# Performance work log

Hardware: AMD Instinct MI355X
Metric: run time of the kernel (lower is better)

Reference implementation:

```python
import jax, jax.numpy as jnp
import numpy as np


def _up(x, h, w):
    # bicubic (Keys a=-0.5, matching PIL BICUBIC) resize of [B,H,W] -> [B,h,w]
    return jax.image.resize(x, (x.shape[0], h, w), method='cubic')


def setup_inputs() -> dict:
    key = jax.random.key(0)
    ks = jax.random.split(key, 10)
    B = 64
    inp = {
        'cam_256': jax.random.uniform(ks[0], (B, 256, 256), dtype=jnp.float32),
        'cam_128': jax.random.uniform(ks[1], (B, 128, 128), dtype=jnp.float32),
        'cam_64':  jax.random.uniform(ks[2], (B, 64, 64), dtype=jnp.float32),
        'cam_32':  jax.random.uniform(ks[3], (B, 32, 32), dtype=jnp.float32),
        'w1': jax.random.normal(ks[4], (2,), dtype=jnp.float32),
        'b1': jax.random.normal(ks[5], (1,), dtype=jnp.float32),
        'w2': jax.random.normal(ks[6], (2,), dtype=jnp.float32),
        'b2': jax.random.normal(ks[7], (1,), dtype=jnp.float32),
        'w3': jax.random.normal(ks[8], (2,), dtype=jnp.float32),
        'b3': jax.random.normal(ks[9], (1,), dtype=jnp.float32),
    }
    return inp


def reference(cam_256, cam_128, cam_64, cam_32, w1, b1, w2, b2, w3, b3):
    B = cam_32.shape[0]
    # stage 1: up(32->64), concat with cam_64, 1x1 conv(2->1) + ReLU
    up32 = _up(cam_32, 64, 64)                              # [B,64,64]
    h64 = jax.nn.relu(w1[0] * up32 + w1[1] * cam_64 + b1[0])
    # stage 2: up(64->128), concat with cam_128, 1x1 conv + ReLU
    up64 = _up(h64, 128, 128)
    h128 = jax.nn.relu(w2[0] * up64 + w2[1] * cam_128 + b2[0])
    # stage 3: up(128->256), concat with cam_256, 1x1 conv + ReLU
    up128 = _up(h128, 256, 256)
    h256 = jax.nn.relu(w3[0] * up128 + w3[1] * cam_256 + b3[0])
    # final: bicubic up to 1024; original loop prepends each new image,
    # reversing batch order -> replicate with flip
    out = _up(h256, 1024, 1024)                             # [B,1024,1024]
    out = jnp.flip(out, axis=0)[:, None]                    # [B,1,1024,1024]
    return out
```

## Files before the change

### kernel.cpp

```cpp
#include <hip/hip_runtime.h>

typedef float vfloat4 __attribute__((ext_vector_type(4)));
typedef float vfloat2 __attribute__((ext_vector_type(2)));

template <bool B> struct BoolC { static constexpr bool value = B; };

__device__ __forceinline__ int iclamp(int v, int lo, int hi) {
  return v < lo ? lo : (v > hi ? hi : v);
}

__device__ __forceinline__ void taps4w(int i, int n, float inv, float w[4]) {
  float s = ((float)i + 0.5f) * inv - 0.5f;
  int k0 = (int)floorf(s);
  float sum = 0.f;
#pragma unroll
  for (int t = 0; t < 4; ++t) {
    int j = k0 - 1 + t;
    float d = fabsf(s - (float)j);
    float wt = (d <= 1.f) ? (((1.5f * d - 2.5f) * d) * d + 1.f)
                          : (((-0.5f * d + 2.5f) * d - 4.f) * d + 2.f);
    if (j < 0 || j >= n) wt = 0.f;
    w[t] = wt;
    sum += wt;
  }
  float r = 1.f / sum;
#pragma unroll
  for (int t = 0; t < 4; ++t) w[t] *= r;
}

#define W0_0 (-0.0439453125f)
#define W0_1 ( 0.3896484375f)
#define W0_2 ( 0.7275390625f)
#define W0_3 (-0.0732421875f)
#define W1_0 (-0.0068359375f)
#define W1_1 ( 0.0908203125f)
#define W1_2 ( 0.9638671875f)
#define W1_3 (-0.0478515625f)
#define U_0 (-0.0234375f)
#define U_1 ( 0.2265625f)
#define U_2 ( 0.8671875f)
#define U_3 (-0.0703125f)

__device__ __forceinline__ void up2_cell(const float (&f)[5][5], int k, int g, int n,
                                         float (&o)[2][2]) {
  if (g >= 2 && g <= n - 3 && k >= 2 && k <= n - 3) {
    float v0[5], v1[5];
#pragma unroll
    for (int c = 0; c < 5; ++c) {
      v0[c] = U_0 * f[0][c] + U_1 * f[1][c] + U_2 * f[2][c] + U_3 * f[3][c];
      v1[c] = U_3 * f[1][c] + U_2 * f[2][c] + U_1 * f[3][c] + U_0 * f[4][c];
    }
    o[0][0] = U_0 * v0[0] + U_1 * v0[1] + U_2 * v0[2] + U_3 * v0[3];
    o[0][1] = U_3 * v0[1] + U_2 * v0[2] + U_1 * v0[3] + U_0 * v0[4];
    o[1][0] = U_0 * v1[0] + U_1 * v1[1] + U_2 * v1[2] + U_3 * v1[3];
    o[1][1] = U_3 * v1[1] + U_2 * v1[2] + U_1 * v1[3] + U_0 * v1[4];
  } else {
#pragma unroll
    for (int p = 0; p < 2; ++p) {
      float wy[4];
      taps4w(2 * k + p, n, 0.5f, wy);
      float vv[5];
#pragma unroll
      for (int c = 0; c < 5; ++c)
        vv[c] = wy[0] * f[p][c] + wy[1] * f[p + 1][c] + wy[2] * f[p + 2][c] + wy[3] * f[p + 3][c];
#pragma unroll
      for (int q = 0; q < 2; ++q) {
        float wx[4];
        taps4w(2 * g + q, n, 0.5f, wx);
        o[p][q] = wx[0] * vv[q] + wx[1] * vv[q + 1] + wx[2] * vv[q + 2] + wx[3] * vv[q + 3];
      }
    }
  }
}

__global__ void __launch_bounds__(256, 4) fused_all(
    const float* __restrict__ cam256, const float* __restrict__ cam128,
    const float* __restrict__ cam64, const float* __restrict__ cam32,
    const float* __restrict__ w1, const float* __restrict__ b1,
    const float* __restrict__ w2, const float* __restrict__ b2,
    const float* __restrict__ w3, const float* __restrict__ b3,
    float* __restrict__ out) {
  __shared__ float s_h64[12 * 64];
  __shared__ float s_h128[16 * 128];
  __shared__ float s_h256[20 * 256];

  const int tid = threadIdx.x;
  const int slab = blockIdx.x;
  const int b = blockIdx.y;
  const int s = slab * 16;

  const int r_lo = s - 2 < 0 ? 0 : s - 2, r_hi = s + 17 > 255 ? 255 : s + 17;
  const int kr0 = r_lo >> 1, kr1 = r_hi >> 1;
  const int h256_row0 = 2 * kr0;
  const int j_lo = kr0 - 2 < 0 ? 0 : kr0 - 2, j_hi = kr1 + 2 > 127 ? 127 : kr1 + 2;
  const int kj0 = j_lo >> 1, kj1 = j_hi >> 1;
  const int h128_row0 = 2 * kj0;
  const int m_lo = kj0 - 2 < 0 ? 0 : kj0 - 2, m_hi = kj1 + 2 > 63 ? 63 : kj1 + 2;
  const int km0 = m_lo >> 1, km1 = m_hi >> 1;
  const int h64_row0 = 2 * km0;

  const float w1_0 = w1[0], w1_1 = w1[1], b1_0 = b1[0];
  const float w2_0 = w2[0], w2_1 = w2[1], b2_0 = b2[0];
  const float w3_0 = w3[0], w3_1 = w3[1], b3_0 = b3[0];

  {
    const float* c32 = cam32 + (size_t)b * 32 * 32;
    const float* c64 = cam64 + (size_t)b * 64 * 64;
    const int nk = km1 - km0 + 1;
    for (int idx = tid; idx < nk * 32; idx += 256) {
      int k = km0 + (idx >> 5), g = idx & 31;
      float f[5][5];
#pragma unroll
      for (int i = 0; i < 5; ++i) {
        int r = iclamp(k - 2 + i, 0, 31);
#pragma unroll
        for (int c = 0; c < 5; ++c) f[i][c] = c32[r * 32 + iclamp(g - 2 + c, 0, 31)];
      }
      float o[2][2];
      up2_cell(f, k, g, 32, o);
#pragma unroll
      for (int p = 0; p < 2; ++p)
#pragma unroll
        for (int q = 0; q < 2; ++q) {
          int row = 2 * k + p, col = 2 * g + q;
          float h = w1_0 * o[p][q] + w1_1 * c64[row * 64 + col] + b1_0;
          s_h64[(row - h64_row0) * 64 + col] = fmaxf(h, 0.f);
        }
    }
  }
  __syncthreads();

  {
    const float* c128 = cam128 + (size_t)b * 128 * 128;
    const int nk = kj1 - kj0 + 1;
    for (int idx = tid; idx < nk * 64; idx += 256) {
      int k = kj0 + (idx >> 6), g = idx & 63;
      float f[5][5];
#pragma unroll
      for (int i = 0; i < 5; ++i) {
        int r = iclamp(k - 2 + i, 0, 63) - h64_row0;
#pragma unroll
        for (int c = 0; c < 5; ++c) f[i][c] = s_h64[r * 64 + iclamp(g - 2 + c, 0, 63)];
      }
      float o[2][2];
      up2_cell(f, k, g, 64, o);
#pragma unroll
      for (int p = 0; p < 2; ++p)
#pragma unroll
        for (int q = 0; q < 2; ++q) {
          int row = 2 * k + p, col = 2 * g + q;
          float h = w2_0 * o[p][q] + w2_1 * c128[row * 128 + col] + b2_0;
          s_h128[(row - h128_row0) * 128 + col] = fmaxf(h, 0.f);
        }
    }
  }
  __syncthreads();

  {
    const float* c256 = cam256 + (size_t)b * 256 * 256;
    const int gc = tid & 127;
    const int sub = tid >> 7;
    const int nk = kr1 - kr0 + 1;
    const int len = (nk + 1) >> 1;
    const int ks = kr0 + sub * len;
    int ke = ks + len - 1;
    if (ke > kr1) ke = kr1;
    if (ks <= kr1) {
      const int cc0 = iclamp(gc - 2, 0, 127), cc1 = iclamp(gc - 1, 0, 127), cc2 = gc,
                cc3 = iclamp(gc + 1, 0, 127), cc4 = iclamp(gc + 2, 0, 127);
      float wa0, wa1, wa2, wa3, wb0, wb1, wb2, wb3;
      if (gc >= 2 && gc <= 125) {
        wa0 = U_0; wa1 = U_1; wa2 = U_2; wa3 = U_3;
        wb0 = U_3; wb1 = U_2; wb2 = U_1; wb3 = U_0;
      } else {
        float ta[4], tb[4];
        taps4w(2 * gc, 128, 0.5f, ta);
        taps4w(2 * gc + 1, 128, 0.5f, tb);
        wa0 = ta[0]; wa1 = ta[1]; wa2 = ta[2]; wa3 = ta[3];
        wb0 = tb[0]; wb1 = tb[1]; wb2 = tb[2]; wb3 = tb[3];
      }
#define H128_ROW_HX(RCLAMP, DST)                                                \
      {                                                                         \
        const float* rp_ = s_h128 + ((RCLAMP) - h128_row0) * 128;               \
        float f0_ = rp_[cc0], f1_ = rp_[cc1], f2_ = rp_[cc2], f3_ = rp_[cc3],   \
              f4_ = rp_[cc4];                                                   \
        DST[0] = wa0 * f0_ + wa1 * f1_ + wa2 * f2_ + wa3 * f3_;                 \
        DST[1] = wb0 * f1_ + wb1 * f2_ + wb2 * f3_ + wb3 * f4_;                 \
      }
      float hx[5][2];
#pragma unroll
      for (int w = 0; w < 5; ++w) {
        int rc = iclamp(ks - 2 + w, 0, 127);
        H128_ROW_HX(rc, hx[w]);
      }
      for (int k = ks; k <= ke; ++k) {
        if (k > ks) {
#pragma unroll
          for (int w = 0; w < 4; ++w) { hx[w][0] = hx[w + 1][0]; hx[w][1] = hx[w + 1][1]; }
          int rc = iclamp(k + 2, 0, 127);
          H128_ROW_HX(rc, hx[4]);
        }
        float p0w[4], p1w[4];
        if (k < 2 || k > 125) {
          taps4w(2 * k, 128, 0.5f, p0w);
          taps4w(2 * k + 1, 128, 0.5f, p1w);
        } else {
          p0w[0] = U_0; p0w[1] = U_1; p0w[2] = U_2; p0w[3] = U_3;
          p1w[0] = U_3; p1w[1] = U_2; p1w[2] = U_1; p1w[3] = U_0;
        }
        float o00 = p0w[0] * hx[0][0] + p0w[1] * hx[1][0] + p0w[2] * hx[2][0] + p0w[3] * hx[3][0];
        float o01 = p0w[0] * hx[0][1] + p0w[1] * hx[1][1] + p0w[2] * hx[2][1] + p0w[3] * hx[3][1];
        float o10 = p1w[0] * hx[1][0] + p1w[1] * hx[2][0] + p1w[2] * hx[3][0] + p1w[3] * hx[4][0];
        float o11 = p1w[0] * hx[1][1] + p1w[1] * hx[2][1] + p1w[2] * hx[3][1] + p1w[3] * hx[4][1];
        const int row0 = 2 * k, col = 2 * gc;
        vfloat2 ca = *(const vfloat2*)(c256 + (size_t)row0 * 256 + col);
        vfloat2 cb = *(const vfloat2*)(c256 + (size_t)(row0 + 1) * 256 + col);
        vfloat2 h0 = {fmaxf(w3_0 * o00 + w3_1 * ca.x + b3_0, 0.f),
                      fmaxf(w3_0 * o01 + w3_1 * ca.y + b3_0, 0.f)};
        vfloat2 h1 = {fmaxf(w3_0 * o10 + w3_1 * cb.x + b3_0, 0.f),
                      fmaxf(w3_0 * o11 + w3_1 * cb.y + b3_0, 0.f)};
        *(vfloat2*)(&s_h256[(row0 - h256_row0) * 256 + col]) = h0;
        *(vfloat2*)(&s_h256[(row0 + 1 - h256_row0) * 256 + col]) = h1;
      }
#undef H128_ROW_HX
    }
  }
  __syncthreads();

  {
    float* outimg = out + (size_t)(63 - b) * 1024 * 1024;
    const int g = tid;
    const int kbase = s;
    const int cc0 = iclamp(g - 2, 0, 255), cc1 = iclamp(g - 1, 0, 255), cc2 = g,
              cc3 = iclamp(g + 1, 0, 255), cc4 = iclamp(g + 2, 0, 255);
    float wx00, wx01, wx02, wx03, wx10, wx11, wx12, wx13;
    float wx20, wx21, wx22, wx23, wx30, wx31, wx32, wx33;
    if (g >= 2 && g <= 253) {
      wx00 = W0_0; wx01 = W0_1; wx02 = W0_2; wx03 = W0_3;
      wx10 = W1_0; wx11 = W1_1; wx12 = W1_2; wx13 = W1_3;
      wx20 = W1_3; wx21 = W1_2; wx22 = W1_1; wx23 = W1_0;
      wx30 = W0_3; wx31 = W0_2; wx32 = W0_1; wx33 = W0_0;
    } else {
      float t0[4], t1[4], t2[4], t3[4];
      taps4w(4 * g + 0, 256, 0.25f, t0);
      taps4w(4 * g + 1, 256, 0.25f, t1);
      taps4w(4 * g + 2, 256, 0.25f, t2);
      taps4w(4 * g + 3, 256, 0.25f, t3);
      wx00 = t0[0]; wx01 = t0[1]; wx02 = t0[2]; wx03 = t0[3];
      wx10 = t1[0]; wx11 = t1[1]; wx12 = t1[2]; wx13 = t1[3];
      wx20 = t2[0]; wx21 = t2[1]; wx22 = t2[2]; wx23 = t2[3];
      wx30 = t3[0]; wx31 = t3[1]; wx32 = t3[2]; wx33 = t3[3];
    }
#define H256_ROW_HX(RCLAMP, DST)                                                \
    {                                                                           \
      const float* rp_ = s_h256 + ((RCLAMP) - h256_row0) * 256;                 \
      float f0_ = rp_[cc0], f1_ = rp_[cc1], f2_ = rp_[cc2], f3_ = rp_[cc3],     \
            f4_ = rp_[cc4];                                                     \
      DST[0] = wx00 * f0_ + wx01 * f1_ + wx02 * f2_ + wx03 * f3_;               \
      DST[1] = wx10 * f0_ + wx11 * f1_ + wx12 * f2_ + wx13 * f3_;               \
      DST[2] = wx20 * f1_ + wx21 * f2_ + wx22 * f3_ + wx23 * f4_;               \
      DST[3] = wx30 * f1_ + wx31 * f2_ + wx32 * f3_ + wx33 * f4_;               \
    }
    auto phaseD = [&](auto bndc) {
      constexpr bool BND = decltype(bndc)::value;
      float hx[5][4];
#pragma unroll
      for (int w = 0; w < 5; ++w) {
        int rc = iclamp(kbase - 2 + w, 0, 255);
        H256_ROW_HX(rc, hx[w]);
      }
      float* op = outimg + (size_t)4 * kbase * 1024 + 4 * g;
#pragma unroll
      for (int step = 0; step < 16; ++step) {
        const int k = kbase + step;
        if (step) {
#pragma unroll
          for (int w = 0; w < 4; ++w)
#pragma unroll
            for (int q = 0; q < 4; ++q) hx[w][q] = hx[w + 1][q];
          int rc = iclamp(k + 2, 0, 255);
          H256_ROW_HX(rc, hx[4]);
        }
        float wy0[4], wy1[4], wy2[4], wy3[4];
        const bool maybe_bnd = BND && ((step < 2) || (step >= 14));
        if (maybe_bnd && (k < 2 || k > 253)) {
          taps4w(4 * k + 0, 256, 0.25f, wy0);
          taps4w(4 * k + 1, 256, 0.25f, wy1);
          taps4w(4 * k + 2, 256, 0.25f, wy2);
          taps4w(4 * k + 3, 256, 0.25f, wy3);
        } else {
          wy0[0] = W0_0; wy0[1] = W0_1; wy0[2] = W0_2; wy0[3] = W0_3;
          wy1[0] = W1_0; wy1[1] = W1_1; wy1[2] = W1_2; wy1[3] = W1_3;
          wy2[0] = W1_3; wy2[1] = W1_2; wy2[2] = W1_1; wy2[3] = W1_0;
          wy3[0] = W0_3; wy3[1] = W0_2; wy3[2] = W0_1; wy3[3] = W0_0;
        }
        vfloat4 v0, v1, v2, v3;
#pragma unroll
        for (int q = 0; q < 4; ++q) {
          v0[q] = wy0[0] * hx[0][q] + wy0[1] * hx[1][q] + wy0[2] * hx[2][q] + wy0[3] * hx[3][q];
          v1[q] = wy1[0] * hx[0][q] + wy1[1] * hx[1][q] + wy1[2] * hx[2][q] + wy1[3] * hx[3][q];
          v2[q] = wy2[0] * hx[1][q] + wy2[1] * hx[2][q] + wy2[2] * hx[3][q] + wy2[3] * hx[4][q];
          v3[q] = wy3[0] * hx[1][q] + wy3[1] * hx[2][q] + wy3[2] * hx[3][q] + wy3[3] * hx[4][q];
        }
        float* rp = op + (size_t)step * 4096;
        *(vfloat4*)(rp) = v0;
        *(vfloat4*)(rp + 1024) = v1;
        *(vfloat4*)(rp + 2048) = v2;
        *(vfloat4*)(rp + 3072) = v3;
      }
    };
    if (slab == 0 || slab == 15) phaseD(BoolC<true>{});
    else phaseD(BoolC<false>{});
#undef H256_ROW_HX
  }
}

extern "C" void kernel_launch(void* const* d_in, const int* in_sizes, int n_in_,
                              void* d_out, int out_size, void* d_ws, size_t ws_size,
                              hipStream_t stream) {
  const float* cam256 = (const float*)d_in[0];
  const float* cam128 = (const float*)d_in[1];
  const float* cam64  = (const float*)d_in[2];
  const float* cam32  = (const float*)d_in[3];
  const float* w1 = (const float*)d_in[4];
  const float* b1 = (const float*)d_in[5];
  const float* w2 = (const float*)d_in[6];
  const float* b2 = (const float*)d_in[7];
  const float* w3 = (const float*)d_in[8];
  const float* b3 = (const float*)d_in[9];
  float* out = (float*)d_out;

  fused_all<<<dim3(16, 64), 256, 0, stream>>>(cam256, cam128, cam64, cam32,
                                              w1, b1, w2, b2, w3, b3, out);
}
```

Measured before the change: 296.0 us.

## Split fused pyramid kernel into h256 producer and streaming 4x upsample kernel

Splits the single fused kernel into two launches. The first computes the 256x256 intermediate per image slab and writes it to workspace. The second streams the final 4x bicubic upsample with a much larger grid (64x64 blocks), reading h256 from global memory and writing vector float4 output rows. This aims to improve parallelism and store bandwidth for the dominant 1024x1024 output write. It costs an extra 16MB round trip and a second launch, and it falls back to the fused kernel when no workspace is provided.

```diff
diff --git a/kernel.cpp b/kernel.cpp
--- a/kernel.cpp
+++ b/kernel.cpp
@@ -71,6 +71,244 @@
       }
     }
   }
+}
+
+__global__ void __launch_bounds__(256, 4) produce_h256(
+    const float* __restrict__ cam256, const float* __restrict__ cam128,
+    const float* __restrict__ cam64, const float* __restrict__ cam32,
+    const float* __restrict__ w1, const float* __restrict__ b1,
+    const float* __restrict__ w2, const float* __restrict__ b2,
+    const float* __restrict__ w3, const float* __restrict__ b3,
+    float* __restrict__ h256g) {
+  __shared__ float s_h64[12 * 64];
+  __shared__ float s_h128[16 * 128];
+
+  const int tid = threadIdx.x;
+  const int slab = blockIdx.x;
+  const int b = blockIdx.y;
+  const int s = slab * 16;
+
+  const int kr0 = s >> 1, kr1 = (s >> 1) + 7;
+  const int j_lo = kr0 - 2 < 0 ? 0 : kr0 - 2, j_hi = kr1 + 2 > 127 ? 127 : kr1 + 2;
+  const int kj0 = j_lo >> 1, kj1 = j_hi >> 1;
+  const int h128_row0 = 2 * kj0;
+  const int m_lo = kj0 - 2 < 0 ? 0 : kj0 - 2, m_hi = kj1 + 2 > 63 ? 63 : kj1 + 2;
+  const int km0 = m_lo >> 1, km1 = m_hi >> 1;
+  const int h64_row0 = 2 * km0;
+
+  const float w1_0 = w1[0], w1_1 = w1[1], b1_0 = b1[0];
+  const float w2_0 = w2[0], w2_1 = w2[1], b2_0 = b2[0];
+  const float w3_0 = w3[0], w3_1 = w3[1], b3_0 = b3[0];
+
+  {
+    const float* c32 = cam32 + (size_t)b * 32 * 32;
+    const float* c64 = cam64 + (size_t)b * 64 * 64;
+    const int nk = km1 - km0 + 1;
+    for (int idx = tid; idx < nk * 32; idx += 256) {
+      int k = km0 + (idx >> 5), g = idx & 31;
+      float f[5][5];
+#pragma unroll
+      for (int i = 0; i < 5; ++i) {
+        int r = iclamp(k - 2 + i, 0, 31);
+#pragma unroll
+        for (int c = 0; c < 5; ++c) f[i][c] = c32[r * 32 + iclamp(g - 2 + c, 0, 31)];
+      }
+      float o[2][2];
+      up2_cell(f, k, g, 32, o);
+#pragma unroll
+      for (int p = 0; p < 2; ++p)
+#pragma unroll
+        for (int q = 0; q < 2; ++q) {
+          int row = 2 * k + p, col = 2 * g + q;
+          float h = w1_0 * o[p][q] + w1_1 * c64[row * 64 + col] + b1_0;
+          s_h64[(row - h64_row0) * 64 + col] = fmaxf(h, 0.f);
+        }
+    }
+  }
+  __syncthreads();
+
+  {
+    const float* c128 = cam128 + (size_t)b * 128 * 128;
+    const int nk = kj1 - kj0 + 1;
+    for (int idx = tid; idx < nk * 64; idx += 256) {
+      int k = kj0 + (idx >> 6), g = idx & 63;
+      float f[5][5];
+#pragma unroll
+      for (int i = 0; i < 5; ++i) {
+        int r = iclamp(k - 2 + i, 0, 63) - h64_row0;
+#pragma unroll
+        for (int c = 0; c < 5; ++c) f[i][c] = s_h64[r * 64 + iclamp(g - 2 + c, 0, 63)];
+      }
+      float o[2][2];
+      up2_cell(f, k, g, 64, o);
+#pragma unroll
+      for (int p = 0; p < 2; ++p)
+#pragma unroll
+        for (int q = 0; q < 2; ++q) {
+          int row = 2 * k + p, col = 2 * g + q;
+          float h = w2_0 * o[p][q] + w2_1 * c128[row * 128 + col] + b2_0;
+          s_h128[(row - h128_row0) * 128 + col] = fmaxf(h, 0.f);
+        }
+    }
+  }
+  __syncthreads();
+
+  {
+    const float* c256 = cam256 + (size_t)b * 256 * 256;
+    float* hg = h256g + (size_t)b * 256 * 256;
+    const int gc = tid & 127;
+    const int sub = tid >> 7;
+    const int ks = kr0 + sub * 4;
+    const int ke = ks + 3;
+    const int cc0 = iclamp(gc - 2, 0, 127), cc1 = iclamp(gc - 1, 0, 127), cc2 = gc,
+              cc3 = iclamp(gc + 1, 0, 127), cc4 = iclamp(gc + 2, 0, 127);
+    float wa0, wa1, wa2, wa3, wb0, wb1, wb2, wb3;
+    if (gc >= 2 && gc <= 125) {
+      wa0 = U_0; wa1 = U_1; wa2 = U_2; wa3 = U_3;
+      wb0 = U_3; wb1 = U_2; wb2 = U_1; wb3 = U_0;
+    } else {
+      float ta[4], tb[4];
+      taps4w(2 * gc, 128, 0.5f, ta);
+      taps4w(2 * gc + 1, 128, 0.5f, tb);
+      wa0 = ta[0]; wa1 = ta[1]; wa2 = ta[2]; wa3 = ta[3];
+      wb0 = tb[0]; wb1 = tb[1]; wb2 = tb[2]; wb3 = tb[3];
+    }
+#define H128_ROW_HX(RCLAMP, DST)                                                \
+    {                                                                           \
+      const float* rp_ = s_h128 + ((RCLAMP) - h128_row0) * 128;                 \
+      float f0_ = rp_[cc0], f1_ = rp_[cc1], f2_ = rp_[cc2], f3_ = rp_[cc3],     \
+            f4_ = rp_[cc4];                                                     \
+      DST[0] = wa0 * f0_ + wa1 * f1_ + wa2 * f2_ + wa3 * f3_;                   \
+      DST[1] = wb0 * f1_ + wb1 * f2_ + wb2 * f3_ + wb3 * f4_;                   \
+    }
+    float hx[5][2];
+#pragma unroll
+    for (int w = 0; w < 5; ++w) {
+      int rc = iclamp(ks - 2 + w, 0, 127);
+      H128_ROW_HX(rc, hx[w]);
+    }
+    for (int k = ks; k <= ke; ++k) {
+      if (k > ks) {
+#pragma unroll
+        for (int w = 0; w < 4; ++w) { hx[w][0] = hx[w + 1][0]; hx[w][1] = hx[w + 1][1]; }
+        int rc = iclamp(k + 2, 0, 127);
+        H128_ROW_HX(rc, hx[4]);
+      }
+      float p0w[4], p1w[4];
+      if (k < 2 || k > 125) {
+        taps4w(2 * k, 128, 0.5f, p0w);
+        taps4w(2 * k + 1, 128, 0.5f, p1w);
+      } else {
+        p0w[0] = U_0; p0w[1] = U_1; p0w[2] = U_2; p0w[3] = U_3;
+        p1w[0] = U_3; p1w[1] = U_2; p1w[2] = U_1; p1w[3] = U_0;
+      }
+      float o00 = p0w[0] * hx[0][0] + p0w[1] * hx[1][0] + p0w[2] * hx[2][0] + p0w[3] * hx[3][0];
+      float o01 = p0w[0] * hx[0][1] + p0w[1] * hx[1][1] + p0w[2] * hx[2][1] + p0w[3] * hx[3][1];
+      float o10 = p1w[0] * hx[1][0] + p1w[1] * hx[2][0] + p1w[2] * hx[3][0] + p1w[3] * hx[4][0];
+      float o11 = p1w[0] * hx[1][1] + p1w[1] * hx[2][1] + p1w[2] * hx[3][1] + p1w[3] * hx[4][1];
+      const int row0 = 2 * k, col = 2 * gc;
+      vfloat2 ca = *(const vfloat2*)(c256 + (size_t)row0 * 256 + col);
+      vfloat2 cb = *(const vfloat2*)(c256 + (size_t)(row0 + 1) * 256 + col);
+      vfloat2 h0 = {fmaxf(w3_0 * o00 + w3_1 * ca.x + b3_0, 0.f),
+                    fmaxf(w3_0 * o01 + w3_1 * ca.y + b3_0, 0.f)};
+      vfloat2 h1 = {fmaxf(w3_0 * o10 + w3_1 * cb.x + b3_0, 0.f),
+                    fmaxf(w3_0 * o11 + w3_1 * cb.y + b3_0, 0.f)};
+      *(vfloat2*)(hg + (size_t)row0 * 256 + col) = h0;
+      *(vfloat2*)(hg + (size_t)(row0 + 1) * 256 + col) = h1;
+    }
+#undef H128_ROW_HX
+  }
+}
+
+__global__ void __launch_bounds__(256, 4) up4_stream(
+    const float* __restrict__ h256g, float* __restrict__ out) {
+  const int g = threadIdx.x;
+  const int sx = blockIdx.x;
+  const int b = blockIdx.y;
+  const float* img = h256g + (size_t)b * 256 * 256;
+  float* outimg = out + (size_t)(63 - b) * 1024 * 1024;
+  const int kbase = sx * 4;
+
+  const int cc0 = iclamp(g - 2, 0, 255), cc1 = iclamp(g - 1, 0, 255), cc2 = g,
+            cc3 = iclamp(g + 1, 0, 255), cc4 = iclamp(g + 2, 0, 255);
+  float wx00, wx01, wx02, wx03, wx10, wx11, wx12, wx13;
+  float wx20, wx21, wx22, wx23, wx30, wx31, wx32, wx33;
+  if (g >= 2 && g <= 253) {
+    wx00 = W0_0; wx01 = W0_1; wx02 = W0_2; wx03 = W0_3;
+    wx10 = W1_0; wx11 = W1_1; wx12 = W1_2; wx13 = W1_3;
+    wx20 = W1_3; wx21 = W1_2; wx22 = W1_1; wx23 = W1_0;
+    wx30 = W0_3; wx31 = W0_2; wx32 = W0_1; wx33 = W0_0;
+  } else {
+    float t0[4], t1[4], t2[4], t3[4];
+    taps4w(4 * g + 0, 256, 0.25f, t0);
+    taps4w(4 * g + 1, 256, 0.25f, t1);
+    taps4w(4 * g + 2, 256, 0.25f, t2);
+    taps4w(4 * g + 3, 256, 0.25f, t3);
+    wx00 = t0[0]; wx01 = t0[1]; wx02 = t0[2]; wx03 = t0[3];
+    wx10 = t1[0]; wx11 = t1[1]; wx12 = t1[2]; wx13 = t1[3];
+    wx20 = t2[0]; wx21 = t2[1]; wx22 = t2[2]; wx23 = t2[3];
+    wx30 = t3[0]; wx31 = t3[1]; wx32 = t3[2]; wx33 = t3[3];
+  }
+#define G256_ROW_HX(RCLAMP, DST)                                                \
+  {                                                                             \
+    const float* rp_ = img + (size_t)(RCLAMP) * 256;                            \
+    float f0_ = rp_[cc0], f1_ = rp_[cc1], f2_ = rp_[cc2], f3_ = rp_[cc3],       \
+          f4_ = rp_[cc4];                                                       \
+    DST[0] = wx00 * f0_ + wx01 * f1_ + wx02 * f2_ + wx03 * f3_;                 \
+    DST[1] = wx10 * f0_ + wx11 * f1_ + wx12 * f2_ + wx13 * f3_;                 \
+    DST[2] = wx20 * f1_ + wx21 * f2_ + wx22 * f3_ + wx23 * f4_;                 \
+    DST[3] = wx30 * f1_ + wx31 * f2_ + wx32 * f3_ + wx33 * f4_;                 \
+  }
+  auto body = [&](auto bndc) {
+    constexpr bool BND = decltype(bndc)::value;
+    float hx[5][4];
+#pragma unroll
+    for (int w = 0; w < 5; ++w) {
+      int rc = iclamp(kbase - 2 + w, 0, 255);
+      G256_ROW_HX(rc, hx[w]);
+    }
+    float* op = outimg + (size_t)4 * kbase * 1024 + 4 * g;
+#pragma unroll
+    for (int step = 0; step < 4; ++step) {
+      const int k = kbase + step;
+      if (step) {
+#pragma unroll
+        for (int w = 0; w < 4; ++w)
+#pragma unroll
+          for (int q = 0; q < 4; ++q) hx[w][q] = hx[w + 1][q];
+        int rc = iclamp(k + 2, 0, 255);
+        G256_ROW_HX(rc, hx[4]);
+      }
+      float wy0[4], wy1[4], wy2[4], wy3[4];
+      if (BND && (k < 2 || k > 253)) {
+        taps4w(4 * k + 0, 256, 0.25f, wy0);
+        taps4w(4 * k + 1, 256, 0.25f, wy1);
+        taps4w(4 * k + 2, 256, 0.25f, wy2);
+        taps4w(4 * k + 3, 256, 0.25f, wy3);
+      } else {
+        wy0[0] = W0_0; wy0[1] = W0_1; wy0[2] = W0_2; wy0[3] = W0_3;
+        wy1[0] = W1_0; wy1[1] = W1_1; wy1[2] = W1_2; wy1[3] = W1_3;
+        wy2[0] = W1_3; wy2[1] = W1_2; wy2[2] = W1_1; wy2[3] = W1_0;
+        wy3[0] = W0_3; wy3[1] = W0_2; wy3[2] = W0_1; wy3[3] = W0_0;
+      }
+      vfloat4 v0, v1, v2, v3;
+#pragma unroll
+      for (int q = 0; q < 4; ++q) {
+        v0[q] = wy0[0] * hx[0][q] + wy0[1] * hx[1][q] + wy0[2] * hx[2][q] + wy0[3] * hx[3][q];
+        v1[q] = wy1[0] * hx[0][q] + wy1[1] * hx[1][q] + wy1[2] * hx[2][q] + wy1[3] * hx[3][q];
+        v2[q] = wy2[0] * hx[1][q] + wy2[1] * hx[2][q] + wy2[2] * hx[3][q] + wy2[3] * hx[4][q];
+        v3[q] = wy3[0] * hx[1][q] + wy3[1] * hx[2][q] + wy3[2] * hx[3][q] + wy3[3] * hx[4][q];
+      }
+      float* rp = op + (size_t)step * 4096;
+      *(vfloat4*)(rp) = v0;
+      *(vfloat4*)(rp + 1024) = v1;
+      *(vfloat4*)(rp + 2048) = v2;
+      *(vfloat4*)(rp + 3072) = v3;
+    }
+  };
+  if (sx == 0 || sx == 63) body(BoolC<true>{});
+  else body(BoolC<false>{});
+#undef G256_ROW_HX
 }
 
 __global__ void __launch_bounds__(256, 4) fused_all(
@@ -330,6 +568,14 @@
   const float* b3 = (const float*)d_in[9];
   float* out = (float*)d_out;
 
-  fused_all<<<dim3(16, 64), 256, 0, stream>>>(cam256, cam128, cam64, cam32,
-                                              w1, b1, w2, b2, w3, b3, out);
-}
+  const size_t need = (size_t)64 * 256 * 256 * sizeof(float);
+  if (d_ws != nullptr && ws_size >= need) {
+    float* h256g = (float*)d_ws;
+    produce_h256<<<dim3(16, 64), 256, 0, stream>>>(cam256, cam128, cam64, cam32,
+                                                   w1, b1, w2, b2, w3, b3, h256g);
+    up4_stream<<<dim3(64, 64), 256, 0, stream>>>(h256g, out);
+  } else {
+    fused_all<<<dim3(16, 64), 256, 0, stream>>>(cam256, cam128, cam64, cam32,
+                                                w1, b1, w2, b2, w3, b3, out);
+  }
+}
```

New measurement: 297.6 us. No clear change (+0.6%).

## Split final 4x upsample into horizontal pass to global buffer and vertical kernels

Applied to the files above, without the earlier changes.

The single fused kernel is split in two stages. The first kernel computes the 256x256 feature rows and their horizontal 4x upsample, without halo rows, into a 64MB global intermediate. Separate boundary and interior kernels then do the vertical pass from that buffer with constant weights on the interior, using more blocks. This removes the redundant halo recomputation and gives the final write stage more parallelism. In exchange it adds a 64MB intermediate write and read plus two extra launches.

```diff
diff --git a/kernel.cpp b/kernel.cpp
--- a/kernel.cpp
+++ b/kernel.cpp
@@ -3,7 +3,7 @@
 typedef float vfloat4 __attribute__((ext_vector_type(4)));
 typedef float vfloat2 __attribute__((ext_vector_type(2)));
 
-template <bool B> struct BoolC { static constexpr bool value = B; };
+__device__ float g_H[(size_t)64 * 256 * 1024];
 
 __device__ __forceinline__ int iclamp(int v, int lo, int hi) {
   return v < lo ? lo : (v > hi ? hi : v);
@@ -73,25 +73,22 @@
   }
 }
 
-__global__ void __launch_bounds__(256, 4) fused_all(
+__global__ void __launch_bounds__(256, 4) produce_H(
     const float* __restrict__ cam256, const float* __restrict__ cam128,
     const float* __restrict__ cam64, const float* __restrict__ cam32,
     const float* __restrict__ w1, const float* __restrict__ b1,
     const float* __restrict__ w2, const float* __restrict__ b2,
-    const float* __restrict__ w3, const float* __restrict__ b3,
-    float* __restrict__ out) {
+    const float* __restrict__ w3, const float* __restrict__ b3) {
   __shared__ float s_h64[12 * 64];
   __shared__ float s_h128[16 * 128];
-  __shared__ float s_h256[20 * 256];
+  __shared__ float s_h256[16 * 256];
 
   const int tid = threadIdx.x;
   const int slab = blockIdx.x;
   const int b = blockIdx.y;
   const int s = slab * 16;
 
-  const int r_lo = s - 2 < 0 ? 0 : s - 2, r_hi = s + 17 > 255 ? 255 : s + 17;
-  const int kr0 = r_lo >> 1, kr1 = r_hi >> 1;
-  const int h256_row0 = 2 * kr0;
+  const int kr0 = s >> 1, kr1 = kr0 + 7;
   const int j_lo = kr0 - 2 < 0 ? 0 : kr0 - 2, j_hi = kr1 + 2 > 127 ? 127 : kr1 + 2;
   const int kj0 = j_lo >> 1, kj1 = j_hi >> 1;
   const int h128_row0 = 2 * kj0;
@@ -160,77 +157,71 @@
     const float* c256 = cam256 + (size_t)b * 256 * 256;
     const int gc = tid & 127;
     const int sub = tid >> 7;
-    const int nk = kr1 - kr0 + 1;
-    const int len = (nk + 1) >> 1;
-    const int ks = kr0 + sub * len;
-    int ke = ks + len - 1;
-    if (ke > kr1) ke = kr1;
-    if (ks <= kr1) {
-      const int cc0 = iclamp(gc - 2, 0, 127), cc1 = iclamp(gc - 1, 0, 127), cc2 = gc,
-                cc3 = iclamp(gc + 1, 0, 127), cc4 = iclamp(gc + 2, 0, 127);
-      float wa0, wa1, wa2, wa3, wb0, wb1, wb2, wb3;
-      if (gc >= 2 && gc <= 125) {
-        wa0 = U_0; wa1 = U_1; wa2 = U_2; wa3 = U_3;
-        wb0 = U_3; wb1 = U_2; wb2 = U_1; wb3 = U_0;
+    const int ks = kr0 + sub * 4;
+    const int ke = ks + 3;
+    const int cc0 = iclamp(gc - 2, 0, 127), cc1 = iclamp(gc - 1, 0, 127), cc2 = gc,
+              cc3 = iclamp(gc + 1, 0, 127), cc4 = iclamp(gc + 2, 0, 127);
+    float wa0, wa1, wa2, wa3, wb0, wb1, wb2, wb3;
+    if (gc >= 2 && gc <= 125) {
+      wa0 = U_0; wa1 = U_1; wa2 = U_2; wa3 = U_3;
+      wb0 = U_3; wb1 = U_2; wb2 = U_1; wb3 = U_0;
+    } else {
+      float ta[4], tb[4];
+      taps4w(2 * gc, 128, 0.5f, ta);
+      taps4w(2 * gc + 1, 128, 0.5f, tb);
+      wa0 = ta[0]; wa1 = ta[1]; wa2 = ta[2]; wa3 = ta[3];
+      wb0 = tb[0]; wb1 = tb[1]; wb2 = tb[2]; wb3 = tb[3];
+    }
+#define H128_ROW_HX(RCLAMP, DST)                                                \
+    {                                                                           \
+      const float* rp_ = s_h128 + ((RCLAMP) - h128_row0) * 128;                 \
+      float f0_ = rp_[cc0], f1_ = rp_[cc1], f2_ = rp_[cc2], f3_ = rp_[cc3],     \
+            f4_ = rp_[cc4];                                                     \
+      DST[0] = wa0 * f0_ + wa1 * f1_ + wa2 * f2_ + wa3 * f3_;                   \
+      DST[1] = wb0 * f1_ + wb1 * f2_ + wb2 * f3_ + wb3 * f4_;                   \
+    }
+    float hx[5][2];
+#pragma unroll
+    for (int w = 0; w < 5; ++w) {
+      int rc = iclamp(ks - 2 + w, 0, 127);
+      H128_ROW_HX(rc, hx[w]);
+    }
+    for (int k = ks; k <= ke; ++k) {
+      if (k > ks) {
+#pragma unroll
+        for (int w = 0; w < 4; ++w) { hx[w][0] = hx[w + 1][0]; hx[w][1] = hx[w + 1][1]; }
+        int rc = iclamp(k + 2, 0, 127);
+        H128_ROW_HX(rc, hx[4]);
+      }
+      float p0w[4], p1w[4];
+      if (k < 2 || k > 125) {
+        taps4w(2 * k, 128, 0.5f, p0w);
+        taps4w(2 * k + 1, 128, 0.5f, p1w);
       } else {
-        float ta[4], tb[4];
-        taps4w(2 * gc, 128, 0.5f, ta);
-        taps4w(2 * gc + 1, 128, 0.5f, tb);
-        wa0 = ta[0]; wa1 = ta[1]; wa2 = ta[2]; wa3 = ta[3];
-        wb0 = tb[0]; wb1 = tb[1]; wb2 = tb[2]; wb3 = tb[3];
-      }
-#define H128_ROW_HX(RCLAMP, DST)                                                \
-      {                                                                         \
-        const float* rp_ = s_h128 + ((RCLAMP) - h128_row0) * 128;               \
-        float f0_ = rp_[cc0], f1_ = rp_[cc1], f2_ = rp_[cc2], f3_ = rp_[cc3],   \
-              f4_ = rp_[cc4];                                                   \
-        DST[0] = wa0 * f0_ + wa1 * f1_ + wa2 * f2_ + wa3 * f3_;                 \
-        DST[1] = wb0 * f1_ + wb1 * f2_ + wb2 * f3_ + wb3 * f4_;                 \
-      }
-      float hx[5][2];
-#pragma unroll
-      for (int w = 0; w < 5; ++w) {
-        int rc = iclamp(ks - 2 + w, 0, 127);
-        H128_ROW_HX(rc, hx[w]);
-      }
-      for (int k = ks; k <= ke; ++k) {
-        if (k > ks) {
-#pragma unroll
-          for (int w = 0; w < 4; ++w) { hx[w][0] = hx[w + 1][0]; hx[w][1] = hx[w + 1][1]; }
-          int rc = iclamp(k + 2, 0, 127);
-          H128_ROW_HX(rc, hx[4]);
-        }
-        float p0w[4], p1w[4];
-        if (k < 2 || k > 125) {
-          taps4w(2 * k, 128, 0.5f, p0w);
-          taps4w(2 * k + 1, 128, 0.5f, p1w);
-        } else {
-          p0w[0] = U_0; p0w[1] = U_1; p0w[2] = U_2; p0w[3] = U_3;
-          p1w[0] = U_3; p1w[1] = U_2; p1w[2] = U_1; p1w[3] = U_0;
-        }
-        float o00 = p0w[0] * hx[0][0] + p0w[1] * hx[1][0] + p0w[2] * hx[2][0] + p0w[3] * hx[3][0];
-        float o01 = p0w[0] * hx[0][1] + p0w[1] * hx[1][1] + p0w[2] * hx[2][1] + p0w[3] * hx[3][1];
-        float o10 = p1w[0] * hx[1][0] + p1w[1] * hx[2][0] + p1w[2] * hx[3][0] + p1w[3] * hx[4][0];
-        float o11 = p1w[0] * hx[1][1] + p1w[1] * hx[2][1] + p1w[2] * hx[3][1] + p1w[3] * hx[4][1];
-        const int row0 = 2 * k, col = 2 * gc;
-        vfloat2 ca = *(const vfloat2*)(c256 + (size_t)row0 * 256 + col);
-        vfloat2 cb = *(const vfloat2*)(c256 + (size_t)(row0 + 1) * 256 + col);
-        vfloat2 h0 = {fmaxf(w3_0 * o00 + w3_1 * ca.x + b3_0, 0.f),
-                      fmaxf(w3_0 * o01 + w3_1 * ca.y + b3_0, 0.f)};
-        vfloat2 h1 = {fmaxf(w3_0 * o10 + w3_1 * cb.x + b3_0, 0.f),
-                      fmaxf(w3_0 * o11 + w3_1 * cb.y + b3_0, 0.f)};
-        *(vfloat2*)(&s_h256[(row0 - h256_row0) * 256 + col]) = h0;
-        *(vfloat2*)(&s_h256[(row0 + 1 - h256_row0) * 256 + col]) = h1;
-      }
+        p0w[0] = U_0; p0w[1] = U_1; p0w[2] = U_2; p0w[3] = U_3;
+        p1w[0] = U_3; p1w[1] = U_2; p1w[2] = U_1; p1w[3] = U_0;
+      }
+      float o00 = p0w[0] * hx[0][0] + p0w[1] * hx[1][0] + p0w[2] * hx[2][0] + p0w[3] * hx[3][0];
+      float o01 = p0w[0] * hx[0][1] + p0w[1] * hx[1][1] + p0w[2] * hx[2][1] + p0w[3] * hx[3][1];
+      float o10 = p1w[0] * hx[1][0] + p1w[1] * hx[2][0] + p1w[2] * hx[3][0] + p1w[3] * hx[4][0];
+      float o11 = p1w[0] * hx[1][1] + p1w[1] * hx[2][1] + p1w[2] * hx[3][1] + p1w[3] * hx[4][1];
+      const int row0 = 2 * k, col = 2 * gc;
+      vfloat2 ca = *(const vfloat2*)(c256 + (size_t)row0 * 256 + col);
+      vfloat2 cb = *(const vfloat2*)(c256 + (size_t)(row0 + 1) * 256 + col);
+      vfloat2 h0 = {fmaxf(w3_0 * o00 + w3_1 * ca.x + b3_0, 0.f),
+                    fmaxf(w3_0 * o01 + w3_1 * ca.y + b3_0, 0.f)};
+      vfloat2 h1 = {fmaxf(w3_0 * o10 + w3_1 * cb.x + b3_0, 0.f),
+                    fmaxf(w3_0 * o11 + w3_1 * cb.y + b3_0, 0.f)};
+      *(vfloat2*)(&s_h256[(row0 - s) * 256 + col]) = h0;
+      *(vfloat2*)(&s_h256[(row0 + 1 - s) * 256 + col]) = h1;
+    }
 #undef H128_ROW_HX
-    }
   }
   __syncthreads();
 
   {
-    float* outimg = out + (size_t)(63 - b) * 1024 * 1024;
+    float* Himg = g_H + (size_t)b * 256 * 1024;
     const int g = tid;
-    const int kbase = s;
     const int cc0 = iclamp(g - 2, 0, 255), cc1 = iclamp(g - 1, 0, 255), cc2 = g,
               cc3 = iclamp(g + 1, 0, 255), cc4 = iclamp(g + 2, 0, 255);
     float wx00, wx01, wx02, wx03, wx10, wx11, wx12, wx13;
@@ -251,67 +242,92 @@
       wx20 = t2[0]; wx21 = t2[1]; wx22 = t2[2]; wx23 = t2[3];
       wx30 = t3[0]; wx31 = t3[1]; wx32 = t3[2]; wx33 = t3[3];
     }
-#define H256_ROW_HX(RCLAMP, DST)                                                \
-    {                                                                           \
-      const float* rp_ = s_h256 + ((RCLAMP) - h256_row0) * 256;                 \
-      float f0_ = rp_[cc0], f1_ = rp_[cc1], f2_ = rp_[cc2], f3_ = rp_[cc3],     \
-            f4_ = rp_[cc4];                                                     \
-      DST[0] = wx00 * f0_ + wx01 * f1_ + wx02 * f2_ + wx03 * f3_;               \
-      DST[1] = wx10 * f0_ + wx11 * f1_ + wx12 * f2_ + wx13 * f3_;               \
-      DST[2] = wx20 * f1_ + wx21 * f2_ + wx22 * f3_ + wx23 * f4_;               \
-      DST[3] = wx30 * f1_ + wx31 * f2_ + wx32 * f3_ + wx33 * f4_;               \
-    }
-    auto phaseD = [&](auto bndc) {
-      constexpr bool BND = decltype(bndc)::value;
-      float hx[5][4];
-#pragma unroll
-      for (int w = 0; w < 5; ++w) {
-        int rc = iclamp(kbase - 2 + w, 0, 255);
-        H256_ROW_HX(rc, hx[w]);
-      }
-      float* op = outimg + (size_t)4 * kbase * 1024 + 4 * g;
-#pragma unroll
-      for (int step = 0; step < 16; ++step) {
-        const int k = kbase + step;
-        if (step) {
-#pragma unroll
-          for (int w = 0; w < 4; ++w)
-#pragma unroll
-            for (int q = 0; q < 4; ++q) hx[w][q] = hx[w + 1][q];
-          int rc = iclamp(k + 2, 0, 255);
-          H256_ROW_HX(rc, hx[4]);
-        }
-        float wy0[4], wy1[4], wy2[4], wy3[4];
-        const bool maybe_bnd = BND && ((step < 2) || (step >= 14));
-        if (maybe_bnd && (k < 2 || k > 253)) {
-          taps4w(4 * k + 0, 256, 0.25f, wy0);
-          taps4w(4 * k + 1, 256, 0.25f, wy1);
-          taps4w(4 * k + 2, 256, 0.25f, wy2);
-          taps4w(4 * k + 3, 256, 0.25f, wy3);
-        } else {
-          wy0[0] = W0_0; wy0[1] = W0_1; wy0[2] = W0_2; wy0[3] = W0_3;
-          wy1[0] = W1_0; wy1[1] = W1_1; wy1[2] = W1_2; wy1[3] = W1_3;
-          wy2[0] = W1_3; wy2[1] = W1_2; wy2[2] = W1_1; wy2[3] = W1_0;
-          wy3[0] = W0_3; wy3[1] = W0_2; wy3[2] = W0_1; wy3[3] = W0_0;
-        }
-        vfloat4 v0, v1, v2, v3;
-#pragma unroll
-        for (int q = 0; q < 4; ++q) {
-          v0[q] = wy0[0] * hx[0][q] + wy0[1] * hx[1][q] + wy0[2] * hx[2][q] + wy0[3] * hx[3][q];
-          v1[q] = wy1[0] * hx[0][q] + wy1[1] * hx[1][q] + wy1[2] * hx[2][q] + wy1[3] * hx[3][q];
-          v2[q] = wy2[0] * hx[1][q] + wy2[1] * hx[2][q] + wy2[2] * hx[3][q] + wy2[3] * hx[4][q];
-          v3[q] = wy3[0] * hx[1][q] + wy3[1] * hx[2][q] + wy3[2] * hx[3][q] + wy3[3] * hx[4][q];
-        }
-        float* rp = op + (size_t)step * 4096;
-        *(vfloat4*)(rp) = v0;
-        *(vfloat4*)(rp + 1024) = v1;
-        *(vfloat4*)(rp + 2048) = v2;
-        *(vfloat4*)(rp + 3072) = v3;
-      }
-    };
-    if (slab == 0 || slab == 15) phaseD(BoolC<true>{});
-    else phaseD(BoolC<false>{});
-#undef H256_ROW_HX
+#pragma unroll 4
+    for (int r = 0; r < 16; ++r) {
+      const float* rp = s_h256 + r * 256;
+      float f0 = rp[cc0], f1 = rp[cc1], f2 = rp[cc2], f3 = rp[cc3], f4 = rp[cc4];
+      vfloat4 v;
+      v[0] = wx00 * f0 + wx01 * f1 + wx02 * f2 + wx03 * f3;
+      v[1] = wx10 * f0 + wx11 * f1 + wx12 * f2 + wx13 * f3;
+      v[2] = wx20 * f1 + wx21 * f2 + wx22 * f3 + wx23 * f4;
+      v[3] = wx30 * f1 + wx31 * f2 + wx32 * f3 + wx33 * f4;
+      *(vfloat4*)(Himg + (size_t)(s + r) * 1024 + 4 * g) = v;
+    }
+  }
+}
+
+__global__ void __launch_bounds__(256, 8) up4_interior(float* __restrict__ out) {
+  const int g = threadIdx.x;
+  const int sx = 1 + (int)blockIdx.x;
+  const int b = blockIdx.y;
+  const int kk0 = sx * 8;
+  const float* hp = g_H + (size_t)b * 256 * 1024 + 4 * g;
+  float* op0 = out + (size_t)(63 - b) * 1024 * 1024 + 4 * g;
+
+  vfloat4 h[5];
+#pragma unroll
+  for (int i = 0; i < 5; ++i)
+    h[i] = *(const vfloat4*)(hp + (size_t)(kk0 - 2 + i) * 1024);
+
+#pragma unroll
+  for (int st = 0; st < 8; ++st) {
+    const int k = kk0 + st;
+    vfloat4 h0 = h[(st + 0) % 5], h1 = h[(st + 1) % 5], h2 = h[(st + 2) % 5],
+            h3 = h[(st + 3) % 5], h4 = h[(st + 4) % 5];
+    vfloat4 v0 = W0_0 * h0 + W0_1 * h1 + W0_2 * h2 + W0_3 * h3;
+    vfloat4 v1 = W1_0 * h0 + W1_1 * h1 + W1_2 * h2 + W1_3 * h3;
+    vfloat4 v2 = W1_3 * h1 + W1_2 * h2 + W1_1 * h3 + W1_0 * h4;
+    vfloat4 v3 = W0_3 * h1 + W0_2 * h2 + W0_1 * h3 + W0_0 * h4;
+    float* rp = op0 + (size_t)(4 * k) * 1024;
+    *(vfloat4*)(rp) = v0;
+    *(vfloat4*)(rp + 1024) = v1;
+    *(vfloat4*)(rp + 2048) = v2;
+    *(vfloat4*)(rp + 3072) = v3;
+    if (st < 7) h[st % 5] = *(const vfloat4*)(hp + (size_t)(k + 3) * 1024);
+  }
+}
+
+__global__ void __launch_bounds__(256, 4) up4_boundary(float* __restrict__ out) {
+  const int g = threadIdx.x;
+  const int sx = (blockIdx.x == 0) ? 0 : 31;
+  const int b = blockIdx.y;
+  const int kk0 = sx * 8;
+  const float* hp = g_H + (size_t)b * 256 * 1024 + 4 * g;
+  float* op0 = out + (size_t)(63 - b) * 1024 * 1024 + 4 * g;
+
+  vfloat4 h[5];
+#pragma unroll
+  for (int i = 0; i < 5; ++i)
+    h[i] = *(const vfloat4*)(hp + (size_t)iclamp(kk0 - 2 + i, 0, 255) * 1024);
+
+#pragma unroll
+  for (int st = 0; st < 8; ++st) {
+    const int k = kk0 + st;
+    vfloat4 h0 = h[(st + 0) % 5], h1 = h[(st + 1) % 5], h2 = h[(st + 2) % 5],
+            h3 = h[(st + 3) % 5], h4 = h[(st + 4) % 5];
+    vfloat4 v0, v1, v2, v3;
+    if (k < 2 || k > 253) {
+      float wy0[4], wy1[4], wy2[4], wy3[4];
+      taps4w(4 * k + 0, 256, 0.25f, wy0);
+      taps4w(4 * k + 1, 256, 0.25f, wy1);
+      taps4w(4 * k + 2, 256, 0.25f, wy2);
+      taps4w(4 * k + 3, 256, 0.25f, wy3);
+      v0 = wy0[0] * h0 + wy0[1] * h1 + wy0[2] * h2 + wy0[3] * h3;
+      v1 = wy1[0] * h0 + wy1[1] * h1 + wy1[2] * h2 + wy1[3] * h3;
+      v2 = wy2[0] * h1 + wy2[1] * h2 + wy2[2] * h3 + wy2[3] * h4;
+      v3 = wy3[0] * h1 + wy3[1] * h2 + wy3[2] * h3 + wy3[3] * h4;
+    } else {
+      v0 = W0_0 * h0 + W0_1 * h1 + W0_2 * h2 + W0_3 * h3;
+      v1 = W1_0 * h0 + W1_1 * h1 + W1_2 * h2 + W1_3 * h3;
+      v2 = W1_3 * h1 + W1_2 * h2 + W1_1 * h3 + W1_0 * h4;
+      v3 = W0_3 * h1 + W0_2 * h2 + W0_1 * h3 + W0_0 * h4;
+    }
+    float* rp = op0 + (size_t)(4 * k) * 1024;
+    *(vfloat4*)(rp) = v0;
+    *(vfloat4*)(rp + 1024) = v1;
+    *(vfloat4*)(rp + 2048) = v2;
+    *(vfloat4*)(rp + 3072) = v3;
+    if (st < 7) h[st % 5] = *(const vfloat4*)(hp + (size_t)iclamp(k + 3, 0, 255) * 1024);
   }
 }
 
@@ -330,6 +346,8 @@
   const float* b3 = (const float*)d_in[9];
   float* out = (float*)d_out;
 
-  fused_all<<<dim3(16, 64), 256, 0, stream>>>(cam256, cam128, cam64, cam32,
-                                              w1, b1, w2, b2, w3, b3, out);
-}
+  produce_H<<<dim3(16, 64), 256, 0, stream>>>(cam256, cam128, cam64, cam32,
+                                              w1, b1, w2, b2, w3, b3);
+  up4_boundary<<<dim3(2, 64), 256, 0, stream>>>(out);
+  up4_interior<<<dim3(30, 64), 256, 0, stream>>>(out);
+}
```

Measured after the change: 327.6 us. 1.11x slower.
